# Kernel optimization log

Measured on AMD Instinct MI355X. Metric: run time of the kernel, lower is better.

Reference implementation:

```python
import jax, jax.numpy as jnp
import numpy as np

EPS = 1e-6
BN_EPS = 1e-5
K = 20

def vn_linear(x, W):
    # x: (B, Cin, 3, ...), W: (Cout, Cin)
    return jnp.einsum('oc,bc...->bo...', W, x)

def vn_batchnorm(x, gamma, beta):
    # x: (B, C, 3, ...). BN (training-mode batch stats) over per-channel vector norms.
    n = jnp.linalg.norm(x, axis=2) + EPS               # (B, C, ...)
    red = (0,) + tuple(range(2, n.ndim))
    mu = n.mean(red, keepdims=True)
    var = ((n - mu) ** 2).mean(red, keepdims=True)     # biased var, as BatchNorm uses
    sh = (1, -1) + (1,) * (n.ndim - 2)
    nbn = (n - mu) / jnp.sqrt(var + BN_EPS) * gamma.reshape(sh) + beta.reshape(sh)
    return x / n[:, :, None] * nbn[:, :, None]

def vn_leaky(x, Wf, Wd, gamma, beta, ns):
    # VNLinearLeakyReLU: linear -> VN batchnorm -> direction-gated leaky relu
    p = vn_batchnorm(vn_linear(x, Wf), gamma, beta)
    d = vn_linear(x, Wd)
    dot = jnp.sum(p * d, axis=2, keepdims=True)
    dsq = jnp.sum(d * d, axis=2, keepdims=True) + EPS
    neg = p - (dot / dsq) * d
    return ns * p + (1.0 - ns) * jnp.where(dot >= 0, p, neg)

def graph_feature_cross(x, k):
    # x: (B, N, 3) -> edge features (B, 3, 3, N, k): [nbr - x, x, nbr x x]
    sq = jnp.sum(x * x, axis=-1)                        # (B, N)
    d2 = sq[:, :, None] + sq[:, None, :] - 2.0 * jnp.einsum('bnd,bmd->bnm', x, x)
    idx = jax.lax.top_k(-d2, k)[1]                      # (B, N, k) nearest incl. self
    nbr = jax.vmap(lambda pts, ind: pts[ind])(x, idx)   # (B, N, k, 3)
    c = jnp.broadcast_to(x[:, :, None, :], nbr.shape)
    cr = jnp.cross(nbr, c)
    feat = jnp.stack([nbr - c, c, cr], axis=3)          # (B, N, k, 3ch, 3)
    return jnp.transpose(feat, (0, 3, 4, 1, 2))         # (B, 3, 3, N, k)


def setup_inputs() -> dict:
    key = jax.random.key(0)
    ks = iter(jax.random.split(key, 40))
    def W(shape):
        return jax.random.normal(next(ks), shape, jnp.float32) * 0.05
    d = {'x': jax.random.normal(next(ks), (2, 2048, 3), jnp.float32)}
    d.update(
        Wf_pos=W((21, 3)), Wd_pos=W((21, 3)), g_pos=jnp.ones(21), be_pos=jnp.zeros(21),
        Wf1=W((21, 21)), Wd1=W((21, 21)), g1=jnp.ones(21), be1=jnp.zeros(21),
        Wf2=W((42, 21)), Wd2=W((42, 21)), g2=jnp.ones(42), be2=jnp.zeros(42),
        W3=W((170, 42)), g3=jnp.ones(170), be3=jnp.zeros(170),
        Ws1f=W((170, 340)), Ws1d=W((170, 340)), gs1=jnp.ones(170), bs1=jnp.zeros(170),
        Ws2f=W((85, 170)), Ws2d=W((85, 170)), gs2=jnp.ones(85), bs2=jnp.zeros(85),
        Wstd=W((3, 85)),
        Wt1=W((1020, 1020)), Wt2=W((1020, 1020)), Wt3=W((14450, 1020)), bt3=jnp.zeros(14450),
    )
    return d


def reference(x, Wf_pos, Wd_pos, g_pos, be_pos, Wf1, Wd1, g1, be1, Wf2, Wd2, g2, be2,
              W3, g3, be3, Ws1f, Ws1d, gs1, bs1, Ws2f, Ws2d, gs2, bs2, Wstd,
              Wt1, Wt2, Wt3, bt3):
    B, N, _ = x.shape
    feat = graph_feature_cross(x, K)                                   # (B,3,3,N,K)
    h = vn_leaky(feat, Wf_pos, Wd_pos, g_pos, be_pos, 0.0).mean(-1)    # (B,21,3,N) pool over k
    h = vn_leaky(h, Wf1, Wd1, g1, be1, 0.0)                            # (B,21,3,N)
    h = vn_leaky(h, Wf2, Wd2, g2, be2, 0.0)                            # (B,42,3,N)
    h = vn_batchnorm(vn_linear(h, W3), g3, be3)                        # (B,170,3,N)
    z = h.mean(-1)                                                     # (B,170,3)
    h = jnp.concatenate([h, jnp.broadcast_to(z[..., None], z.shape + (N,))], axis=1)  # (B,340,3,N)
    # VNStdFeature (normalize_frame=False, default negative_slope=0.2 inside)
    z0 = vn_leaky(h, Ws1f, Ws1d, gs1, bs1, 0.2)                        # (B,170,3,N)
    z0 = vn_leaky(z0, Ws2f, Ws2d, gs2, bs2, 0.2)                       # (B,85,3,N)
    z0 = vn_linear(z0, Wstd)                                           # (B,3,3,N)
    hs = jnp.einsum('bijn,bjkn->bikn', h, z0)                          # (B,340,3,N) invariant feats
    t = hs.reshape(B, 340 * 3, N)                                      # (B,1020,N)
    t = jax.nn.relu(jnp.einsum('oc,bcn->bon', Wt1, t))
    t = jax.nn.relu(jnp.einsum('oc,bcn->bon', Wt2, t))
    t = jnp.einsum('oc,bcn->bon', Wt3, t) + bt3[None, :, None]         # (B,14450,N)
    theta = t.reshape(B, 85, 170, N)
    return (z, theta)
```

## Files before the change

kernel.cpp:

```cpp
#include <hip/hip_runtime.h>
#include <cstdint>
#include <cstddef>

constexpr int   BB     = 2;
constexpr int   NN     = 2048;
constexpr int   KNB    = 20;
constexpr float EPS_   = 1e-6f;
constexpr float BNEPS_ = 1e-5f;
constexpr int   KPAD   = 1024;
constexpr int   NTK    = KPAD / 64;

typedef __bf16 bf16x8 __attribute__((ext_vector_type(8)));
typedef float  f32x4  __attribute__((ext_vector_type(4)));

typedef const void t_gvoid __attribute__((address_space(1)));
typedef void       t_lvoid __attribute__((address_space(3)));

__device__ __forceinline__ unsigned short f2bf(float f) {
  unsigned int u = __builtin_bit_cast(unsigned int, f);
  u += 0x7FFFu + ((u >> 16) & 1u);
  return (unsigned short)(u >> 16);
}

__global__ __launch_bounds__(256) void knn_kernel(const float* __restrict__ x,
                                                  int* __restrict__ idx) {
  __shared__ float4 pts[NN];
  const int b = blockIdx.x >> 9;
  const int tid = threadIdx.x;
  const float* xb = x + (size_t)b * NN * 3;
  for (int i = tid; i < NN; i += 256) {
    float px = xb[i * 3], py = xb[i * 3 + 1], pz = xb[i * 3 + 2];
    pts[i] = make_float4(px, py, pz, px * px + py * py + pz * pz);
  }
  __syncthreads();
  const int wave = tid >> 6, lane = tid & 63;
  const int q = (blockIdx.x & 511) * 4 + wave;
  const float4 qp = pts[q];

  float d[32];
  #pragma unroll
  for (int i = 0; i < 32; ++i) {
    const float4 p = pts[lane + 64 * i];
    d[i] = qp.w + p.w - 2.0f * (qp.x * p.x + qp.y * p.y + qp.z * p.z);
  }

  float m; int mi;
  auto rescan = [&]() {
    m = 3.4e38f; mi = 0;
    #pragma unroll
    for (int i = 0; i < 32; ++i)
      if (d[i] < m) { m = d[i]; mi = i; }
  };
  rescan();

  int* op = idx + ((size_t)b * NN + q) * KNB;
  for (int r = 0; r < KNB; ++r) {
    float bm = m; int bj = lane + 64 * mi;
    #pragma unroll
    for (int s = 32; s > 0; s >>= 1) {
      const float om = __shfl_xor(bm, s, 64);
      const int   oj = __shfl_xor(bj, s, 64);
      if (om < bm || (om == bm && oj < bj)) { bm = om; bj = oj; }
    }
    if (lane == 0) op[r] = bj;
    if ((bj & 63) == lane) {
      const int ii = bj >> 6;
      #pragma unroll
      for (int i = 0; i < 32; ++i)
        if (i == ii) d[i] = 3.4e38f;
      rescan();
    }
  }
}

__global__ void feat_kernel(const float* __restrict__ x, const int* __restrict__ idx,
                            float* __restrict__ feat) {
  const int i = blockIdx.x * 256 + threadIdx.x;
  if (i >= BB * NN * KNB) return;
  const int n = (i / KNB) % NN, b = i / (KNB * NN);
  const float* xb = x + (size_t)b * NN * 3;
  const int j = idx[i];
  const float cx = xb[n * 3], cy = xb[n * 3 + 1], cz = xb[n * 3 + 2];
  const float nx = xb[j * 3], ny = xb[j * 3 + 1], nz = xb[j * 3 + 2];
  float* f = feat + (size_t)i * 9;
  f[0] = nx - cx; f[1] = ny - cy; f[2] = nz - cz;
  f[3] = cx;      f[4] = cy;      f[5] = cz;
  f[6] = ny * cz - nz * cy;
  f[7] = nz * cx - nx * cz;
  f[8] = nx * cy - ny * cx;
}

__global__ void l1_stats_part(const float* __restrict__ feat, const float* __restrict__ Wf,
                              float* __restrict__ part) {
  const int o = blockIdx.x, g = blockIdx.y, tid = threadIdx.x;
  const float w0 = Wf[o * 3], w1 = Wf[o * 3 + 1], w2 = Wf[o * 3 + 2];
  const int M = BB * NN * KNB;
  const int chunk = M / 8;
  float s1 = 0.f, s2 = 0.f;
  for (int i = g * chunk + tid; i < (g + 1) * chunk; i += 256) {
    const float* f = feat + (size_t)i * 9;
    float p0 = w0 * f[0] + w1 * f[3] + w2 * f[6];
    float p1 = w0 * f[1] + w1 * f[4] + w2 * f[7];
    float p2 = w0 * f[2] + w1 * f[5] + w2 * f[8];
    float nr = sqrtf(p0 * p0 + p1 * p1 + p2 * p2) + EPS_;
    s1 += nr; s2 += nr * nr;
  }
  __shared__ float rA[256], rB[256];
  rA[tid] = s1; rB[tid] = s2; __syncthreads();
  for (int off = 128; off > 0; off >>= 1) {
    if (tid < off) { rA[tid] += rA[tid + off]; rB[tid] += rB[tid + off]; }
    __syncthreads();
  }
  if (tid == 0) {
    part[(o * 8 + g) * 2]     = rA[0];
    part[(o * 8 + g) * 2 + 1] = rB[0];
  }
}

__global__ void l1_stats_fin(const float* __restrict__ part, const float* __restrict__ gamma,
                             float* __restrict__ stats) {
  const int o = threadIdx.x;
  if (o >= 21) return;
  const int M = BB * NN * KNB;
  float s1 = 0.f, s2 = 0.f;
  for (int g = 0; g < 8; ++g) { s1 += part[(o * 8 + g) * 2]; s2 += part[(o * 8 + g) * 2 + 1]; }
  float mu = s1 / M;
  float var = fmaxf(s2 / M - mu * mu, 0.f);
  stats[2 * o] = mu;
  stats[2 * o + 1] = gamma[o] / sqrtf(var + BNEPS_);
}

__global__ void l1_final_kernel(const float* __restrict__ feat, const float* __restrict__ Wf,
                                const float* __restrict__ Wd, const float* __restrict__ stats,
                                const float* __restrict__ beta, float* __restrict__ h1) {
  const int o = blockIdx.y, b = blockIdx.z;
  const int n = blockIdx.x * 256 + threadIdx.x;
  const float wf0 = Wf[o * 3], wf1 = Wf[o * 3 + 1], wf2 = Wf[o * 3 + 2];
  const float wd0 = Wd[o * 3], wd1 = Wd[o * 3 + 1], wd2 = Wd[o * 3 + 2];
  const float mu = stats[2 * o], sc = stats[2 * o + 1], be = beta[o];
  const float* fb = feat + ((size_t)(b * NN + n)) * KNB * 9;
  float a0 = 0.f, a1 = 0.f, a2 = 0.f;
  for (int k = 0; k < KNB; ++k) {
    const float* f = fb + k * 9;
    float p0 = wf0 * f[0] + wf1 * f[3] + wf2 * f[6];
    float p1 = wf0 * f[1] + wf1 * f[4] + wf2 * f[7];
    float p2 = wf0 * f[2] + wf1 * f[5] + wf2 * f[8];
    float d0 = wd0 * f[0] + wd1 * f[3] + wd2 * f[6];
    float d1 = wd0 * f[1] + wd1 * f[4] + wd2 * f[7];
    float d2 = wd0 * f[2] + wd1 * f[5] + wd2 * f[8];
    float nr = sqrtf(p0 * p0 + p1 * p1 + p2 * p2) + EPS_;
    float fac = ((nr - mu) * sc + be) / nr;
    p0 *= fac; p1 *= fac; p2 *= fac;
    float dot = p0 * d0 + p1 * d1 + p2 * d2;
    if (dot < 0.f) {
      float g = dot / (d0 * d0 + d1 * d1 + d2 * d2 + EPS_);
      p0 -= g * d0; p1 -= g * d1; p2 -= g * d2;
    }
    a0 += p0; a1 += p1; a2 += p2;
  }
  const size_t base = ((size_t)(b * 21 + o) * 3) * NN + n;
  h1[base]          = a0 * (1.f / KNB);
  h1[base + NN]     = a1 * (1.f / KNB);
  h1[base + 2 * NN] = a2 * (1.f / KNB);
}

__global__ void zbias_kernel(const float* __restrict__ zbuf, const float* __restrict__ Wf,
                             const float* __restrict__ Wd, float* __restrict__ zbf,
                             float* __restrict__ zbd, int Cout, int CinFull, int Cz) {
  const int bj = blockIdx.x;
  const int b = bj / 3, j = bj % 3;
  const int o = threadIdx.x;
  if (o >= Cout) return;
  const int off = CinFull - Cz;
  float sf = 0.f, sd = 0.f;
  for (int cz = 0; cz < Cz; ++cz) {
    const float zv = zbuf[((size_t)b * 170 + cz) * 3 + j];
    sf += Wf[(size_t)o * CinFull + off + cz] * zv;
    sd += Wd[(size_t)o * CinFull + off + cz] * zv;
  }
  zbf[(size_t)bj * Cout + o] = sf;
  zbd[(size_t)bj * Cout + o] = sd;
}

template <int HAS_D, int CONCAT_Z>
__global__ __launch_bounds__(256) void vn_lin_fast(
    const float* __restrict__ in, const float* __restrict__ Wf, const float* __restrict__ Wd,
    const float* __restrict__ zbf, const float* __restrict__ zbd,
    float* __restrict__ pout, float* __restrict__ dout,
    int Cin, int CinFull, int Cout) {
  __shared__ float wsh[(HAS_D ? 2 : 1) * 16 * 340];
  float* wfs = wsh;
  float* wds = HAS_D ? (wsh + 16 * 340) : wsh;
  const int tid = threadIdx.x;
  const int nt = blockIdx.x, ot = blockIdx.y;
  const int b = blockIdx.z / 3, j = blockIdx.z % 3;

  for (int i = tid; i < 16 * Cin; i += 256) {
    const int ol = i / Cin, c = i - ol * Cin;
    const int o = ot * 16 + ol;
    wfs[ol * Cin + c] = (o < Cout) ? Wf[(size_t)o * CinFull + c] : 0.f;
    if (HAS_D) wds[ol * Cin + c] = (o < Cout) ? Wd[(size_t)o * CinFull + c] : 0.f;
  }
  __syncthreads();

  const int lane = tid & 63, og = tid >> 6;
  const int n0 = nt * 256 + lane * 4;
  const float* ibase = in + ((size_t)b * Cin * 3 + j) * NN + n0;

  f32x4 accf[4], accd[4];
  #pragma unroll
  for (int oo = 0; oo < 4; ++oo) {
    float bf = 0.f, bd = 0.f;
    if (CONCAT_Z) {
      const int o = ot * 16 + og * 4 + oo;
      if (o < Cout) {
        bf = zbf[(size_t)blockIdx.z * Cout + o];
        bd = zbd[(size_t)blockIdx.z * Cout + o];
      }
    }
    accf[oo] = (f32x4){bf, bf, bf, bf};
    accd[oo] = (f32x4){bd, bd, bd, bd};
  }

  #pragma unroll 4
  for (int c = 0; c < Cin; ++c) {
    const f32x4 v = *reinterpret_cast<const f32x4*>(ibase + (size_t)c * 3 * NN);
    #pragma unroll
    for (int oo = 0; oo < 4; ++oo) {
      const float wf = wfs[(og * 4 + oo) * Cin + c];
      accf[oo] += wf * v;
      if (HAS_D) {
        const float wd = wds[(og * 4 + oo) * Cin + c];
        accd[oo] += wd * v;
      }
    }
  }

  #pragma unroll
  for (int oo = 0; oo < 4; ++oo) {
    const int o = ot * 16 + og * 4 + oo;
    if (o < Cout) {
      const size_t ob = ((size_t)(b * Cout + o) * 3 + j) * NN + n0;
      *reinterpret_cast<f32x4*>(pout + ob) = accf[oo];
      if (HAS_D) *reinterpret_cast<f32x4*>(dout + ob) = accd[oo];
    }
  }
}

__global__ void bn_stats_kernel(const float* __restrict__ p, const float* __restrict__ gamma,
                                float* __restrict__ stats, int Cout) {
  const int o = blockIdx.x, tid = threadIdx.x;
  const int M = BB * NN;
  float s1 = 0.f, s2 = 0.f;
  for (int i = tid; i < M; i += 256) {
    const int b = i >> 11, n = i & (NN - 1);
    const size_t base = (((size_t)(b * Cout + o)) * 3) * NN + n;
    float p0 = p[base], p1 = p[base + NN], p2 = p[base + 2 * NN];
    float nr = sqrtf(p0 * p0 + p1 * p1 + p2 * p2) + EPS_;
    s1 += nr; s2 += nr * nr;
  }
  __shared__ float rA[256], rB[256];
  rA[tid] = s1; rB[tid] = s2; __syncthreads();
  for (int off = 128; off > 0; off >>= 1) {
    if (tid < off) { rA[tid] += rA[tid + off]; rB[tid] += rB[tid + off]; }
    __syncthreads();
  }
  if (tid == 0) {
    float mu = rA[0] / M;
    float var = fmaxf(rB[0] / M - mu * mu, 0.f);
    stats[2 * o] = mu;
    stats[2 * o + 1] = gamma[o] / sqrtf(var + BNEPS_);
  }
}

template <int GATE>
__global__ void vn_gate_kernel(const float* __restrict__ p, const float* __restrict__ d,
                               const float* __restrict__ stats, const float* __restrict__ beta,
                               float* __restrict__ out, int Cout, float ns) {
  const int o = blockIdx.y, b = blockIdx.z;
  const int n = blockIdx.x * 256 + threadIdx.x;
  const size_t base = (((size_t)(b * Cout + o)) * 3) * NN + n;
  float p0 = p[base], p1 = p[base + NN], p2 = p[base + 2 * NN];
  const float nr = sqrtf(p0 * p0 + p1 * p1 + p2 * p2) + EPS_;
  const float fac = ((nr - stats[2 * o]) * stats[2 * o + 1] + beta[o]) / nr;
  p0 *= fac; p1 *= fac; p2 *= fac;
  float o0 = p0, o1 = p1, o2 = p2;
  if (GATE) {
    const float d0 = d[base], d1 = d[base + NN], d2 = d[base + 2 * NN];
    const float dot = p0 * d0 + p1 * d1 + p2 * d2;
    if (dot < 0.f) {
      const float g = dot / (d0 * d0 + d1 * d1 + d2 * d2 + EPS_);
      o0 = p0 - g * d0; o1 = p1 - g * d1; o2 = p2 - g * d2;
    }
    o0 = ns * p0 + (1.f - ns) * o0;
    o1 = ns * p1 + (1.f - ns) * o1;
    o2 = ns * p2 + (1.f - ns) * o2;
  }
  out[base] = o0; out[base + NN] = o1; out[base + 2 * NN] = o2;
}

__global__ void zmean_kernel(const float* __restrict__ h4, float* __restrict__ zbuf,
                             float* __restrict__ outz) {
  const int oj = blockIdx.x;
  const int b = blockIdx.y;
  const int tid = threadIdx.x;
  const float* src = h4 + ((size_t)b * 510 + oj) * NN;
  float s = 0.f;
  for (int n = tid; n < NN; n += 256) s += src[n];
  __shared__ float r[256];
  r[tid] = s; __syncthreads();
  for (int off = 128; off > 0; off >>= 1) {
    if (tid < off) r[tid] += r[tid + off];
    __syncthreads();
  }
  if (tid == 0) {
    float m = r[0] / NN;
    zbuf[(size_t)b * 510 + oj] = m;
    outz[(size_t)b * 510 + oj] = m;
  }
}

__global__ void hs_kernel(const float* __restrict__ h4, const float* __restrict__ zbuf,
                          const float* __restrict__ z0f, unsigned short* __restrict__ t0) {
  const int n = blockIdx.x;
  const int b = blockIdx.z;
  const int tid = threadIdx.x;
  __shared__ float zf[9];
  if (tid < 9) zf[tid] = z0f[(((size_t)(b * 3 + tid / 3)) * 3 + (tid % 3)) * NN + n];
  __syncthreads();
  unsigned short* trow = t0 + ((size_t)b * NN + n) * KPAD;
  for (int c = tid; c < KPAD; c += 256) {
    if (c >= 1020) { trow[c] = 0; continue; }
    const int i = c / 3, kv = c % 3;
    float acc = 0.f;
    #pragma unroll
    for (int j = 0; j < 3; ++j) {
      float hv = (i < 170) ? h4[(((size_t)(b * 170 + i)) * 3 + j) * NN + n]
                           : zbuf[(size_t)b * 510 + (i - 170) * 3 + j];
      acc += hv * zf[j * 3 + kv];
    }
    trow[c] = f2bf(acc);
  }
}

__global__ void wconv_kernel(const float* __restrict__ W, unsigned short* __restrict__ out,
                             int M, int Kv, size_t total) {
  size_t i = (size_t)blockIdx.x * 256 + threadIdx.x;
  const size_t stride = (size_t)gridDim.x * 256;
  for (; i < total; i += stride) {
    const int k = (int)(i & (KPAD - 1));
    const int o = (int)(i >> 10);
    out[i] = (o < M && k < Kv) ? f2bf(W[(size_t)o * Kv + k]) : (unsigned short)0;
  }
}

template <int RELU, int OUTF32>
__global__ __launch_bounds__(256) void gemm_kernel(
    const unsigned short* __restrict__ A, const unsigned short* __restrict__ Bmat,
    unsigned short* __restrict__ outB, float* __restrict__ outF,
    const float* __restrict__ bias, int M) {
  __shared__ __align__(16) unsigned short lA[2][128 * 64];
  __shared__ __align__(16) unsigned short lB[2][128 * 64];
  const int tid = threadIdx.x;
  const int ntile = blockIdx.x, mtile = blockIdx.y, b = blockIdx.z;
  const int lane = tid & 63, w = tid >> 6;
  const int wm = w >> 1, wn = w & 1;
  const int lrow = lane & 15, lgrp = lane >> 4;

  const unsigned short* Abase = A + (size_t)mtile * 128 * KPAD;
  const unsigned short* Bbase = Bmat + ((size_t)b * NN + (size_t)ntile * 128) * KPAD;

  const int rowS = tid >> 3;
  const int scol = ((tid & 7) * 8) ^ ((rowS & 7) * 8);
  const int wb8  = __builtin_amdgcn_readfirstlane(tid & 192) * 8;

  f32x4 acc[4][4];
  #pragma unroll
  for (int mi = 0; mi < 4; ++mi)
    #pragma unroll
    for (int ni = 0; ni < 4; ++ni) acc[mi][ni] = (f32x4){0.f, 0.f, 0.f, 0.f};

  auto stage = [&](int bufi, int kt) {
    const int kof = kt * 64;
    #pragma unroll
    for (int r = 0; r < 4; ++r) {
      __builtin_amdgcn_global_load_lds(
          (t_gvoid*)(Abase + (size_t)(r * 32 + rowS) * KPAD + kof + scol),
          (t_lvoid*)&lA[bufi][r * 2048 + wb8], 16, 0, 0);
      __builtin_amdgcn_global_load_lds(
          (t_gvoid*)(Bbase + (size_t)(r * 32 + rowS) * KPAD + kof + scol),
          (t_lvoid*)&lB[bufi][r * 2048 + wb8], 16, 0, 0);
    }
  };

  stage(0, 0);
  for (int kt = 0; kt < NTK; ++kt) {
    const int cur = kt & 1;
    if (kt + 1 < NTK) {
      stage(cur ^ 1, kt + 1);
      asm volatile("s_waitcnt vmcnt(8)" ::: "memory");
    } else {
      asm volatile("s_waitcnt vmcnt(0)" ::: "memory");
    }
    asm volatile("s_barrier" ::: "memory");

    bf16x8 af[4][2], bfr[4][2];
    #pragma unroll
    for (int mi = 0; mi < 4; ++mi) {
      const int ra = wm * 64 + mi * 16 + lrow;
      const int rb = wn * 64 + mi * 16 + lrow;
      #pragma unroll
      for (int kk = 0; kk < 2; ++kk) {
        af[mi][kk]  = *reinterpret_cast<const bf16x8*>(
            &lA[cur][ra * 64 + ((kk * 32 + lgrp * 8) ^ ((ra & 7) * 8))]);
        bfr[mi][kk] = *reinterpret_cast<const bf16x8*>(
            &lB[cur][rb * 64 + ((kk * 32 + lgrp * 8) ^ ((rb & 7) * 8))]);
      }
    }
    #pragma unroll
    for (int kk = 0; kk < 2; ++kk)
      #pragma unroll
      for (int mi = 0; mi < 4; ++mi)
        #pragma unroll
        for (int ni = 0; ni < 4; ++ni)
          acc[mi][ni] = __builtin_amdgcn_mfma_f32_16x16x32_bf16(af[mi][kk], bfr[ni][kk],
                                                                acc[mi][ni], 0, 0, 0);
    asm volatile("s_barrier" ::: "memory");
  }

  const int fr_col = lane & 15;
  const int fr_rowb = (lane >> 4) * 4;
  #pragma unroll
  for (int mi = 0; mi < 4; ++mi) {
    const int rowb = mtile * 128 + wm * 64 + mi * 16 + fr_rowb;
    #pragma unroll
    for (int ni = 0; ni < 4; ++ni) {
      const int col = ntile * 128 + wn * 64 + ni * 16 + fr_col;
      if (OUTF32) {
        #pragma unroll
        for (int r = 0; r < 4; ++r) {
          const int rr = rowb + r;
          if (rr < M) outF[((size_t)b * M + rr) * NN + col] = acc[mi][ni][r] + bias[rr];
        }
      } else {
        ushort4 v;
        if (rowb < M) {
          float u0 = acc[mi][ni][0], u1 = acc[mi][ni][1], u2 = acc[mi][ni][2], u3 = acc[mi][ni][3];
          if (RELU) { u0 = fmaxf(u0, 0.f); u1 = fmaxf(u1, 0.f); u2 = fmaxf(u2, 0.f); u3 = fmaxf(u3, 0.f); }
          v.x = f2bf(u0); v.y = f2bf(u1); v.z = f2bf(u2); v.w = f2bf(u3);
        } else {
          v.x = v.y = v.z = v.w = 0;
        }
        *reinterpret_cast<ushort4*>(outB + ((size_t)b * NN + col) * KPAD + rowb) = v;
      }
    }
  }
}

extern "C" void kernel_launch(void* const* d_in, const int* in_sizes, int n_in,
                              void* d_out, int out_size, void* d_ws, size_t ws_size,
                              hipStream_t stream) {
  const float* x      = (const float*)d_in[0];
  const float* Wf_pos = (const float*)d_in[1];
  const float* Wd_pos = (const float*)d_in[2];
  const float* g_pos  = (const float*)d_in[3];
  const float* be_pos = (const float*)d_in[4];
  const float* Wf1    = (const float*)d_in[5];
  const float* Wd1    = (const float*)d_in[6];
  const float* g1     = (const float*)d_in[7];
  const float* be1    = (const float*)d_in[8];
  const float* Wf2    = (const float*)d_in[9];
  const float* Wd2    = (const float*)d_in[10];
  const float* g2     = (const float*)d_in[11];
  const float* be2    = (const float*)d_in[12];
  const float* W3     = (const float*)d_in[13];
  const float* g3     = (const float*)d_in[14];
  const float* be3    = (const float*)d_in[15];
  const float* Ws1f   = (const float*)d_in[16];
  const float* Ws1d   = (const float*)d_in[17];
  const float* gs1    = (const float*)d_in[18];
  const float* bs1    = (const float*)d_in[19];
  const float* Ws2f   = (const float*)d_in[20];
  const float* Ws2d   = (const float*)d_in[21];
  const float* gs2    = (const float*)d_in[22];
  const float* bs2    = (const float*)d_in[23];
  const float* Wstd   = (const float*)d_in[24];
  const float* Wt1    = (const float*)d_in[25];
  const float* Wt2    = (const float*)d_in[26];
  const float* Wt3    = (const float*)d_in[27];
  const float* bt3    = (const float*)d_in[28];
  (void)in_sizes; (void)n_in; (void)out_size; (void)ws_size;

  float* out = (float*)d_out;
  float* out_theta = out + 1020;

  char* ws = (char*)d_ws;
  size_t off = 0;
  auto alloc = [&](size_t bytes) -> void* {
    void* p = (void*)(ws + off);
    off += (bytes + 255) & ~(size_t)255;
    return p;
  };
  int*            idx  = (int*)           alloc((size_t)BB * NN * KNB * 4);
  float*          feat = (float*)         alloc((size_t)BB * NN * KNB * 9 * 4);
  float*          stats= (float*)         alloc(1024 * 4);
  float*          part = (float*)         alloc(2048 * 4);
  float*          h1   = (float*)         alloc((size_t)BB * 21 * 3 * NN * 4);
  float*          h2   = (float*)         alloc((size_t)BB * 21 * 3 * NN * 4);
  float*          h3   = (float*)         alloc((size_t)BB * 42 * 3 * NN * 4);
  float*          h4   = (float*)         alloc((size_t)BB * 170 * 3 * NN * 4);
  float*          zbuf = (float*)         alloc((size_t)BB * 170 * 3 * 4);
  float*          pbuf = (float*)         alloc((size_t)BB * 170 * 3 * NN * 4);
  float*          dbuf = (float*)         alloc((size_t)BB * 170 * 3 * NN * 4);
  float*          z0a  = (float*)         alloc((size_t)BB * 170 * 3 * NN * 4);
  float*          z0b  = (float*)         alloc((size_t)BB * 85 * 3 * NN * 4);
  float*          z0f  = (float*)         alloc((size_t)BB * 3 * 3 * NN * 4);
  float*          zbf  = (float*)         alloc((size_t)6 * 170 * 4);
  float*          zbd  = (float*)         alloc((size_t)6 * 170 * 4);
  unsigned short* W1b  = (unsigned short*)alloc((size_t)1024 * KPAD * 2);
  unsigned short* W2b  = (unsigned short*)alloc((size_t)1024 * KPAD * 2);
  unsigned short* W3b  = (unsigned short*)alloc((size_t)14464 * KPAD * 2);
  unsigned short* t0   = (unsigned short*)alloc((size_t)BB * NN * KPAD * 2);
  unsigned short* t1   = (unsigned short*)alloc((size_t)BB * NN * KPAD * 2);
  unsigned short* t2   = t0;

  knn_kernel<<<BB * 512, 256, 0, stream>>>(x, idx);
  feat_kernel<<<(BB * NN * KNB + 255) / 256, 256, 0, stream>>>(x, idx, feat);
  l1_stats_part<<<dim3(21, 8), 256, 0, stream>>>(feat, Wf_pos, part);
  l1_stats_fin<<<1, 64, 0, stream>>>(part, g_pos, stats);
  l1_final_kernel<<<dim3(8, 21, BB), 256, 0, stream>>>(feat, Wf_pos, Wd_pos, stats, be_pos, h1);

  vn_lin_fast<1, 0><<<dim3(8, 2, BB * 3), 256, 0, stream>>>(h1, Wf1, Wd1, nullptr, nullptr, pbuf, dbuf, 21, 21, 21);
  bn_stats_kernel<<<21, 256, 0, stream>>>(pbuf, g1, stats, 21);
  vn_gate_kernel<1><<<dim3(8, 21, BB), 256, 0, stream>>>(pbuf, dbuf, stats, be1, h2, 21, 0.0f);

  vn_lin_fast<1, 0><<<dim3(8, 3, BB * 3), 256, 0, stream>>>(h2, Wf2, Wd2, nullptr, nullptr, pbuf, dbuf, 21, 21, 42);
  bn_stats_kernel<<<42, 256, 0, stream>>>(pbuf, g2, stats, 42);
  vn_gate_kernel<1><<<dim3(8, 42, BB), 256, 0, stream>>>(pbuf, dbuf, stats, be2, h3, 42, 0.0f);

  vn_lin_fast<0, 0><<<dim3(8, 11, BB * 3), 256, 0, stream>>>(h3, W3, nullptr, nullptr, nullptr, pbuf, nullptr, 42, 42, 170);
  bn_stats_kernel<<<170, 256, 0, stream>>>(pbuf, g3, stats, 170);
  vn_gate_kernel<0><<<dim3(8, 170, BB), 256, 0, stream>>>(pbuf, nullptr, stats, be3, h4, 170, 0.0f);

  zmean_kernel<<<dim3(510, BB), 256, 0, stream>>>(h4, zbuf, out);

  zbias_kernel<<<6, 256, 0, stream>>>(zbuf, Ws1f, Ws1d, zbf, zbd, 170, 340, 170);
  vn_lin_fast<1, 1><<<dim3(8, 11, BB * 3), 256, 0, stream>>>(h4, Ws1f, Ws1d, zbf, zbd, pbuf, dbuf, 170, 340, 170);
  bn_stats_kernel<<<170, 256, 0, stream>>>(pbuf, gs1, stats, 170);
  vn_gate_kernel<1><<<dim3(8, 170, BB), 256, 0, stream>>>(pbuf, dbuf, stats, bs1, z0a, 170, 0.2f);

  vn_lin_fast<1, 0><<<dim3(8, 6, BB * 3), 256, 0, stream>>>(z0a, Ws2f, Ws2d, nullptr, nullptr, pbuf, dbuf, 170, 170, 85);
  bn_stats_kernel<<<85, 256, 0, stream>>>(pbuf, gs2, stats, 85);
  vn_gate_kernel<1><<<dim3(8, 85, BB), 256, 0, stream>>>(pbuf, dbuf, stats, bs2, z0b, 85, 0.2f);

  vn_lin_fast<0, 0><<<dim3(8, 1, BB * 3), 256, 0, stream>>>(z0b, Wstd, nullptr, nullptr, nullptr, z0f, nullptr, 85, 85, 3);

  hs_kernel<<<dim3(NN, 1, BB), 256, 0, stream>>>(h4, zbuf, z0f, t0);

  wconv_kernel<<<1024, 256, 0, stream>>>(Wt1, W1b, 1020, 1020, (size_t)1024 * KPAD);
  wconv_kernel<<<1024, 256, 0, stream>>>(Wt2, W2b, 1020, 1020, (size_t)1024 * KPAD);
  wconv_kernel<<<2048, 256, 0, stream>>>(Wt3, W3b, 14450, 1020, (size_t)14464 * KPAD);

  gemm_kernel<1, 0><<<dim3(16, 8, BB), 256, 0, stream>>>(W1b, t0, t1, nullptr, nullptr, 1020);
  gemm_kernel<1, 0><<<dim3(16, 8, BB), 256, 0, stream>>>(W2b, t1, t2, nullptr, nullptr, 1020);
  gemm_kernel<0, 1><<<dim3(16, 113, BB), 256, 0, stream>>>(W3b, t2, nullptr, out_theta, bt3, 14450);
}
```

Before: 602.2 us.

## Use 256x256 tiles for final GEMM and swizzle workgroup order

```diff
diff --git a/kernel.cpp b/kernel.cpp
--- a/kernel.cpp
+++ b/kernel.cpp
@@ -9,6 +9,8 @@
 constexpr float BNEPS_ = 1e-5f;
 constexpr int   KPAD   = 1024;
 constexpr int   NTK    = KPAD / 64;
+constexpr int   MT3    = 57;
+constexpr int   MPAD3  = MT3 * 256;
 
 typedef __bf16 bf16x8 __attribute__((ext_vector_type(8)));
 typedef float  f32x4  __attribute__((ext_vector_type(4)));
@@ -354,15 +356,19 @@
   }
 }
 
-template <int RELU, int OUTF32>
+template <int RELU>
 __global__ __launch_bounds__(256) void gemm_kernel(
     const unsigned short* __restrict__ A, const unsigned short* __restrict__ Bmat,
-    unsigned short* __restrict__ outB, float* __restrict__ outF,
-    const float* __restrict__ bias, int M) {
+    unsigned short* __restrict__ outB, int M) {
   __shared__ __align__(16) unsigned short lA[2][128 * 64];
   __shared__ __align__(16) unsigned short lB[2][128 * 64];
   const int tid = threadIdx.x;
-  const int ntile = blockIdx.x, mtile = blockIdx.y, b = blockIdx.z;
+  const int nwg = gridDim.x, q = nwg >> 3;
+  const int orig = blockIdx.x;
+  const int swz = (orig & 7) * q + (orig >> 3);
+  const int ntile = swz & 15;
+  const int mtile = (swz >> 4) & 7;
+  const int b = swz >> 7;
   const int lane = tid & 63, w = tid >> 6;
   const int wm = w >> 1, wn = w & 1;
   const int lrow = lane & 15, lgrp = lane >> 4;
@@ -436,22 +442,110 @@
     #pragma unroll
     for (int ni = 0; ni < 4; ++ni) {
       const int col = ntile * 128 + wn * 64 + ni * 16 + fr_col;
-      if (OUTF32) {
+      ushort4 v;
+      if (rowb < M) {
+        float u0 = acc[mi][ni][0], u1 = acc[mi][ni][1], u2 = acc[mi][ni][2], u3 = acc[mi][ni][3];
+        if (RELU) { u0 = fmaxf(u0, 0.f); u1 = fmaxf(u1, 0.f); u2 = fmaxf(u2, 0.f); u3 = fmaxf(u3, 0.f); }
+        v.x = f2bf(u0); v.y = f2bf(u1); v.z = f2bf(u2); v.w = f2bf(u3);
+      } else {
+        v.x = v.y = v.z = v.w = 0;
+      }
+      *reinterpret_cast<ushort4*>(outB + ((size_t)b * NN + col) * KPAD + rowb) = v;
+    }
+  }
+}
+
+__global__ __launch_bounds__(512, 2) void gemm256_kernel(
+    const unsigned short* __restrict__ A, const unsigned short* __restrict__ Bmat,
+    float* __restrict__ outF, const float* __restrict__ bias, int M, int MT) {
+  __shared__ __align__(16) unsigned short lA[2][256 * 64];
+  __shared__ __align__(16) unsigned short lB[2][256 * 64];
+  const int tid = threadIdx.x;
+  const int nwg = gridDim.x, q = nwg >> 3;
+  const int orig = blockIdx.x;
+  const int swz = (orig & 7) * q + (orig >> 3);
+  const int ntile = swz & 7;
+  const int rem = swz >> 3;
+  const int mtile = rem % MT;
+  const int b = rem / MT;
+  const int lane = tid & 63, w = tid >> 6;
+  const int wm = w >> 2, wn = w & 3;
+  const int lrow = lane & 15, lgrp = lane >> 4;
+
+  const unsigned short* Abase = A + (size_t)mtile * 256 * KPAD;
+  const unsigned short* Bbase = Bmat + ((size_t)b * NN + (size_t)ntile * 256) * KPAD;
+
+  const int rowS = tid >> 3;
+  const int scol = ((tid & 7) * 8) ^ ((rowS & 7) * 8);
+  const int wb8  = __builtin_amdgcn_readfirstlane((tid & 448) >> 6) * 512;
+
+  f32x4 acc[8][4];
+  #pragma unroll
+  for (int mi = 0; mi < 8; ++mi)
+    #pragma unroll
+    for (int ni = 0; ni < 4; ++ni) acc[mi][ni] = (f32x4){0.f, 0.f, 0.f, 0.f};
+
+  auto stage = [&](int bufi, int kt) {
+    const int kof = kt * 64;
+    #pragma unroll
+    for (int r = 0; r < 4; ++r) {
+      __builtin_amdgcn_global_load_lds(
+          (t_gvoid*)(Abase + (size_t)(r * 64 + rowS) * KPAD + kof + scol),
+          (t_lvoid*)&lA[bufi][r * 4096 + wb8], 16, 0, 0);
+      __builtin_amdgcn_global_load_lds(
+          (t_gvoid*)(Bbase + (size_t)(r * 64 + rowS) * KPAD + kof + scol),
+          (t_lvoid*)&lB[bufi][r * 4096 + wb8], 16, 0, 0);
+    }
+  };
+
+  stage(0, 0);
+  for (int kt = 0; kt < NTK; ++kt) {
+    const int cur = kt & 1;
+    if (kt + 1 < NTK) {
+      stage(cur ^ 1, kt + 1);
+      asm volatile("s_waitcnt vmcnt(8)" ::: "memory");
+    } else {
+      asm volatile("s_waitcnt vmcnt(0)" ::: "memory");
+    }
+    asm volatile("s_barrier" ::: "memory");
+
+    #pragma unroll
+    for (int kk = 0; kk < 2; ++kk) {
+      bf16x8 af[8], bfr[4];
+      #pragma unroll
+      for (int mi = 0; mi < 8; ++mi) {
+        const int ra = wm * 128 + mi * 16 + lrow;
+        af[mi] = *reinterpret_cast<const bf16x8*>(
+            &lA[cur][ra * 64 + ((kk * 32 + lgrp * 8) ^ ((ra & 7) * 8))]);
+      }
+      #pragma unroll
+      for (int ni = 0; ni < 4; ++ni) {
+        const int rb = wn * 64 + ni * 16 + lrow;
+        bfr[ni] = *reinterpret_cast<const bf16x8*>(
+            &lB[cur][rb * 64 + ((kk * 32 + lgrp * 8) ^ ((rb & 7) * 8))]);
+      }
+      #pragma unroll
+      for (int mi = 0; mi < 8; ++mi)
         #pragma unroll
-        for (int r = 0; r < 4; ++r) {
-          const int rr = rowb + r;
-          if (rr < M) outF[((size_t)b * M + rr) * NN + col] = acc[mi][ni][r] + bias[rr];
-        }
-      } else {
-        ushort4 v;
-        if (rowb < M) {
-          float u0 = acc[mi][ni][0], u1 = acc[mi][ni][1], u2 = acc[mi][ni][2], u3 = acc[mi][ni][3];
-          if (RELU) { u0 = fmaxf(u0, 0.f); u1 = fmaxf(u1, 0.f); u2 = fmaxf(u2, 0.f); u3 = fmaxf(u3, 0.f); }
-          v.x = f2bf(u0); v.y = f2bf(u1); v.z = f2bf(u2); v.w = f2bf(u3);
-        } else {
-          v.x = v.y = v.z = v.w = 0;
-        }
-        *reinterpret_cast<ushort4*>(outB + ((size_t)b * NN + col) * KPAD + rowb) = v;
+        for (int ni = 0; ni < 4; ++ni)
+          acc[mi][ni] = __builtin_amdgcn_mfma_f32_16x16x32_bf16(af[mi], bfr[ni],
+                                                                acc[mi][ni], 0, 0, 0);
+    }
+    asm volatile("s_barrier" ::: "memory");
+  }
+
+  const int fr_col = lane & 15;
+  const int fr_rowb = (lane >> 4) * 4;
+  #pragma unroll
+  for (int mi = 0; mi < 8; ++mi) {
+    const int rowb = mtile * 256 + wm * 128 + mi * 16 + fr_rowb;
+    #pragma unroll
+    for (int ni = 0; ni < 4; ++ni) {
+      const int col = ntile * 256 + wn * 64 + ni * 16 + fr_col;
+      #pragma unroll
+      for (int r = 0; r < 4; ++r) {
+        const int rr = rowb + r;
+        if (rr < M) outF[((size_t)b * M + rr) * NN + col] = acc[mi][ni][r] + bias[rr];
       }
     }
   }
@@ -519,7 +613,7 @@
   float*          zbd  = (float*)         alloc((size_t)6 * 170 * 4);
   unsigned short* W1b  = (unsigned short*)alloc((size_t)1024 * KPAD * 2);
   unsigned short* W2b  = (unsigned short*)alloc((size_t)1024 * KPAD * 2);
-  unsigned short* W3b  = (unsigned short*)alloc((size_t)14464 * KPAD * 2);
+  unsigned short* W3b  = (unsigned short*)alloc((size_t)MPAD3 * KPAD * 2);
   unsigned short* t0   = (unsigned short*)alloc((size_t)BB * NN * KPAD * 2);
   unsigned short* t1   = (unsigned short*)alloc((size_t)BB * NN * KPAD * 2);
   unsigned short* t2   = t0;
@@ -559,9 +653,9 @@
 
   wconv_kernel<<<1024, 256, 0, stream>>>(Wt1, W1b, 1020, 1020, (size_t)1024 * KPAD);
   wconv_kernel<<<1024, 256, 0, stream>>>(Wt2, W2b, 1020, 1020, (size_t)1024 * KPAD);
-  wconv_kernel<<<2048, 256, 0, stream>>>(Wt3, W3b, 14450, 1020, (size_t)14464 * KPAD);
-
-  gemm_kernel<1, 0><<<dim3(16, 8, BB), 256, 0, stream>>>(W1b, t0, t1, nullptr, nullptr, 1020);
-  gemm_kernel<1, 0><<<dim3(16, 8, BB), 256, 0, stream>>>(W2b, t1, t2, nullptr, nullptr, 1020);
-  gemm_kernel<0, 1><<<dim3(16, 113, BB), 256, 0, stream>>>(W3b, t2, nullptr, out_theta, bt3, 14450);
-}
+  wconv_kernel<<<2048, 256, 0, stream>>>(Wt3, W3b, 14450, 1020, (size_t)MPAD3 * KPAD);
+
+  gemm_kernel<1><<<256, 256, 0, stream>>>(W1b, t0, t1, 1020);
+  gemm_kernel<1><<<256, 256, 0, stream>>>(W2b, t1, t2, 1020);
+  gemm256_kernel<<<8 * MT3 * BB, 512, 0, stream>>>(W3b, t2, out_theta, bt3, 14450, MT3);
+}
```

Measured after the change: 568.1 us. 5.7% less time.
